# Optimization experiments

Measured on AMD Instinct MI355X. Metric: run time of the kernel, lower is better.

Reference implementation:

```python
import jax, jax.numpy as jnp
import numpy as np

B, T, L, D = 512, 100, 256, 128
DEPTH = 8                 # perfect binary tree depth -> path length DEPTH+1
P = DEPTH + 1
N_PER_TREE = 2 * L - 1    # 511 nodes per tree (heap layout)
N_TOTAL = T * N_PER_TREE  # 51100 global nodes


def _build_paths():
    # Heap layout per tree: internal nodes 0..L-2, leaves L-1..2L-2.
    # Path for leaf l = chain of heap ancestors from root to leaf.
    local = np.zeros((L, P), dtype=np.int32)
    for l in range(L):
        node = L - 1 + l
        chain = []
        while True:
            chain.append(node)
            if node == 0:
                break
            node = (node - 1) // 2
        local[l] = np.array(chain[::-1], dtype=np.int32)
    offs = (np.arange(T, dtype=np.int32) * N_PER_TREE)[:, None, None]
    return local[None, :, :] + offs  # [T, L, P] global node ids


def setup_inputs() -> dict:
    key = jax.random.key(0)
    k1, k2, k3, k4, k5, k6 = jax.random.split(key, 6)
    paths = jnp.asarray(_build_paths())
    # GBDT multi-hot: exactly one activated leaf per tree per sample
    leaf = jax.random.randint(k1, (B, T), 0, L)
    cross = (jnp.zeros((B, T, L), jnp.float32)
             .at[jnp.arange(B)[:, None], jnp.arange(T)[None, :], leaf]
             .set(1.0)
             .reshape(B, T * L))
    s = 1.0 / float(np.sqrt(D))  # torch LSTM init range
    node_emb = jax.random.normal(k2, (N_TOTAL, D), jnp.float32) * 0.01
    w_ih = jax.random.uniform(k3, (4 * D, D), jnp.float32, -s, s)
    w_hh = jax.random.uniform(k4, (4 * D, D), jnp.float32, -s, s)
    b_ih = jax.random.uniform(k5, (4 * D,), jnp.float32, -s, s)
    b_hh = jax.random.uniform(k6, (4 * D,), jnp.float32, -s, s)
    return {"cross_features": cross, "node_emb": node_emb, "w_ih": w_ih,
            "w_hh": w_hh, "b_ih": b_ih, "b_hh": b_hh, "paths": paths}


def _lstm_last_h(x, w_ih, w_hh, b_ih, b_hh):
    # x: [S, P, D] -> final hidden state [S, D]; torch gate order i, f, g, o
    S = x.shape[0]
    d = w_hh.shape[1]
    bias = b_ih + b_hh

    def step(carry, x_t):
        h, c = carry
        g = x_t @ w_ih.T + h @ w_hh.T + bias          # [S, 4D]
        i, f, gg, o = jnp.split(g, 4, axis=-1)
        c = jax.nn.sigmoid(f) * c + jax.nn.sigmoid(i) * jnp.tanh(gg)
        h = jax.nn.sigmoid(o) * jnp.tanh(c)
        return (h, c), None

    h0 = jnp.zeros((S, d), x.dtype)
    (h, _), _ = jax.lax.scan(step, (h0, h0), jnp.swapaxes(x, 0, 1))
    return h


def reference(cross_features, node_emb, w_ih, w_hh, b_ih, b_hh, paths):
    t, l, p = paths.shape
    b = cross_features.shape[0]
    d = node_emb.shape[1]
    cf = cross_features.reshape(b, t, l)
    leaf = jnp.argmax(cf, axis=-1)                    # [B, T] activated leaf per tree
    active = jnp.any(cf > 0, axis=-1)                 # [B, T] tree has an activated leaf
    node_ids = paths[jnp.arange(t)[None, :], leaf]    # [B, T, P] root-to-leaf global ids
    x = node_emb[node_ids].reshape(b * t, p, d)       # batched path gather
    h = _lstm_last_h(x, w_ih, w_hh, b_ih, b_hh).reshape(b, t, d)
    return jnp.where(active[..., None], h, jnp.zeros((), h.dtype))
```

## Files before the change

kernel.cpp:

```cpp
#include <hip/hip_runtime.h>
#include <math.h>


#define B_N 512
#define T_N 100
#define L_N 256
#define D_N 128
#define NPT 511

typedef __attribute__((ext_vector_type(8))) short short8;
typedef __attribute__((ext_vector_type(4))) float f32x4;
typedef __attribute__((ext_vector_type(4))) unsigned short ushort4v;

__device__ __forceinline__ unsigned short f2bf(float f) {
    unsigned u = __float_as_uint(f);
    return (unsigned short)((u + 0x7FFFu + ((u >> 16) & 1u)) >> 16);
}
__device__ __forceinline__ float bf2f(unsigned short b) {
    return __uint_as_float(((unsigned)b) << 16);
}
__device__ __forceinline__ float fsigmoid(float x) {
    return __builtin_amdgcn_rcpf(1.f + __builtin_amdgcn_exp2f(-1.44269504f * x));
}
__device__ __forceinline__ float ftanh(float x) {
    return 1.f - 2.f * __builtin_amdgcn_rcpf(1.f + __builtin_amdgcn_exp2f(2.88539009f * x));
}
__device__ __forceinline__ void keepreg(short8 &x) {
    asm volatile("" : "+v"(x));
}

__global__ __launch_bounds__(256) void pack_kernel(const float* __restrict__ w_ih,
                                                   const float* __restrict__ w_hh,
                                                   const float* __restrict__ b_ih,
                                                   const float* __restrict__ b_hh,
                                                   unsigned short* __restrict__ Bhi,
                                                   unsigned short* __restrict__ Blo,
                                                   float* __restrict__ bias) {
    const int idx = blockIdx.x * 256 + threadIdx.x;
    const int k  = idx & 255;
    const int np = idx >> 8;
    const float val = (k < 128) ? w_ih[(size_t)np * 128 + k]
                                : w_hh[(size_t)np * 128 + (k - 128)];
    const unsigned short hi = f2bf(val);
    const int kb = k >> 5, krel = k & 31, quad = krel >> 3, e = krel & 7;
    const int tn = np >> 4, col = np & 15, lane = quad * 16 + col;
    Bhi[(((size_t)kb * 32 + tn) * 64 + lane) * 8 + e] = hi;
    if (kb >= 4) {
        const unsigned short lo = f2bf(val - bf2f(hi));
        Blo[((((size_t)kb - 4) * 32 + tn) * 64 + lane) * 8 + e] = lo;
    }
    if (k == 0) bias[np] = b_ih[np] + b_hh[np];
}

__global__ __launch_bounds__(512, 2) void tree_kernel(
    const float* __restrict__ node_emb,
    const unsigned short* __restrict__ Bhi,
    const unsigned short* __restrict__ Blo,
    const float* __restrict__ bias,
    float* __restrict__ h8)
{
    __shared__ float hbuf[2][16][132];
    __shared__ float cbuf[2][16][132];
    __shared__ float h7buf[32][132];
    __shared__ float c7buf[32][132];
    __shared__ unsigned short AhiF[8 * 2 * 512];
    __shared__ unsigned short AloF[4 * 2 * 512];

    const int t    = blockIdx.x >> 2;
    const int s    = blockIdx.x & 3;
    const int tid  = threadIdx.x;
    const int idx  = tid >> 6;
    const int lane = tid & 63;
    const int ml   = lane & 15;
    const int quad = lane >> 4;
    const int j    = idx * 16 + ml;

    const float bi = bias[j];
    const float bf = bias[128 + j];
    const float bg = bias[256 + j];
    const float bo = bias[384 + j];

    const short8* Bh8 = reinterpret_cast<const short8*>(Bhi);
    const short8* Bl8 = reinterpret_cast<const short8*>(Blo);
    const short8* Ah8 = reinterpret_cast<const short8*>(AhiF);
    const short8* Al8 = reinterpret_cast<const short8*>(AloF);

    short8 bhR[8][4], blR[4][4];
    #pragma unroll
    for (int kb = 0; kb < 8; ++kb)
        #pragma unroll
        for (int g = 0; g < 4; ++g)
            bhR[kb][g] = Bh8[(kb * 32 + g * 8 + idx) * 64 + lane];
    #pragma unroll
    for (int kb = 0; kb < 4; ++kb)
        #pragma unroll
        for (int g = 0; g < 4; ++g)
            blR[kb][g] = Bl8[(kb * 32 + g * 8 + idx) * 64 + lane];
    #pragma unroll
    for (int kb = 0; kb < 8; ++kb)
        #pragma unroll
        for (int g = 0; g < 4; ++g)
            keepreg(bhR[kb][g]);
    #pragma unroll
    for (int kb = 0; kb < 4; ++kb)
        #pragma unroll
        for (int g = 0; g < 4; ++g)
            keepreg(blR[kb][g]);

    for (int d = 0; d <= 6; ++d) {
        const int Mrows = (d == 0) ? 1 : (d == 1) ? 2 : (1 << (d - 2));
        const int pbase = (d >= 2) ? (s << (d - 2)) : 0;
        const bool root = (d == 0);
        const int cur = d & 1, prv = cur ^ 1;

        #pragma unroll
        for (int h2 = 0; h2 < 2; ++h2) {
            const int r  = tid & 15;
            const int k4 = (tid >> 4) + h2 * 32;
            const int k  = k4 * 4;
            int p = r; if (p > Mrows - 1) p = Mrows - 1;
            float4 v;
            if (k < 128) {
                const int local = (1 << d) - 1 + pbase + p;
                v = *reinterpret_cast<const float4*>(
                        node_emb + (size_t)(t * NPT + local) * D_N + k);
            } else if (root) {
                v = make_float4(0.f, 0.f, 0.f, 0.f);
            } else {
                const int pr = (d == 2) ? (s >> 1) : (p >> 1);
                v = *reinterpret_cast<const float4*>(&hbuf[prv][pr][k - 128]);
            }
            const int kb = k >> 5, qk = (k & 31) >> 3, e0 = k & 4;
            const ushort4v hv = { f2bf(v.x), f2bf(v.y), f2bf(v.z), f2bf(v.w) };
            *reinterpret_cast<ushort4v*>(
                &AhiF[((kb * 2 + 0) * 64 + qk * 16 + r) * 8 + e0]) = hv;
            if (k >= 128) {
                const ushort4v lv = { f2bf(v.x - bf2f(hv.x)), f2bf(v.y - bf2f(hv.y)),
                                      f2bf(v.z - bf2f(hv.z)), f2bf(v.w - bf2f(hv.w)) };
                *reinterpret_cast<ushort4v*>(
                    &AloF[(((kb - 4) * 2 + 0) * 64 + qk * 16 + r) * 8 + e0]) = lv;
            }
        }
        __syncthreads();

        float cpre[4];
        #pragma unroll
        for (int rr = 0; rr < 4; ++rr) {
            int m = quad * 4 + rr;
            if (m > Mrows - 1) m = Mrows - 1;
            const int pr = (d == 2) ? (s >> 1) : (m >> 1);
            cpre[rr] = root ? 0.f : cbuf[prv][pr][j];
        }

        f32x4 acc[4];
        #pragma unroll
        for (int g = 0; g < 4; ++g) acc[g] = (f32x4)0.f;

        #pragma unroll
        for (int kb = 0; kb < 8; ++kb) {
            const short8 ah = Ah8[(kb * 2 + 0) * 64 + lane];
            short8 al;
            if (kb >= 4) al = Al8[((kb - 4) * 2 + 0) * 64 + lane];
            #pragma unroll
            for (int g = 0; g < 4; ++g) {
                acc[g] = __builtin_amdgcn_mfma_f32_16x16x32_bf16(
                    ah, bhR[kb][g], acc[g], 0, 0, 0);
                if (kb >= 4) {
                    acc[g] = __builtin_amdgcn_mfma_f32_16x16x32_bf16(
                        ah, blR[kb - 4][g], acc[g], 0, 0, 0);
                    acc[g] = __builtin_amdgcn_mfma_f32_16x16x32_bf16(
                        al, bhR[kb][g], acc[g], 0, 0, 0);
                }
            }
        }

        #pragma unroll
        for (int rr = 0; rr < 4; ++rr) {
            const int m = quad * 4 + rr;
            if (m < Mrows) {
                const float ig = fsigmoid(acc[0][rr] + bi);
                const float fg = fsigmoid(acc[1][rr] + bf);
                const float gv = ftanh(acc[2][rr] + bg);
                const float og = fsigmoid(acc[3][rr] + bo);
                const float cn = fg * cpre[rr] + ig * gv;
                const float hn = og * ftanh(cn);
                hbuf[cur][m][j] = hn;
                cbuf[cur][m][j] = cn;
            }
        }
        __syncthreads();
    }

    {
        #pragma unroll
        for (int h2 = 0; h2 < 4; ++h2) {
            const int r  = tid & 31;
            const int k4 = (tid >> 5) + h2 * 16;
            const int k  = k4 * 4;
            const int mt = r >> 4, mlr = r & 15;
            float4 v;
            if (k < 128) {
                const int local = 127 + s * 32 + r;
                v = *reinterpret_cast<const float4*>(
                        node_emb + (size_t)(t * NPT + local) * D_N + k);
            } else {
                v = *reinterpret_cast<const float4*>(&hbuf[0][r >> 1][k - 128]);
            }
            const int kb = k >> 5, qk = (k & 31) >> 3, e0 = k & 4;
            const ushort4v hv = { f2bf(v.x), f2bf(v.y), f2bf(v.z), f2bf(v.w) };
            *reinterpret_cast<ushort4v*>(
                &AhiF[((kb * 2 + mt) * 64 + qk * 16 + mlr) * 8 + e0]) = hv;
            if (k >= 128) {
                const ushort4v lv = { f2bf(v.x - bf2f(hv.x)), f2bf(v.y - bf2f(hv.y)),
                                      f2bf(v.z - bf2f(hv.z)), f2bf(v.w - bf2f(hv.w)) };
                *reinterpret_cast<ushort4v*>(
                    &AloF[(((kb - 4) * 2 + mt) * 64 + qk * 16 + mlr) * 8 + e0]) = lv;
            }
        }
        __syncthreads();

        #pragma unroll
        for (int mt = 0; mt < 2; ++mt) {
            float cpre[4];
            #pragma unroll
            for (int rr = 0; rr < 4; ++rr) {
                const int m = mt * 16 + quad * 4 + rr;
                cpre[rr] = cbuf[0][m >> 1][j];
            }
            f32x4 acc[4];
            #pragma unroll
            for (int g = 0; g < 4; ++g) acc[g] = (f32x4)0.f;
            #pragma unroll
            for (int kb = 0; kb < 8; ++kb) {
                const short8 ah = Ah8[(kb * 2 + mt) * 64 + lane];
                short8 al;
                if (kb >= 4) al = Al8[((kb - 4) * 2 + mt) * 64 + lane];
                #pragma unroll
                for (int g = 0; g < 4; ++g) {
                    acc[g] = __builtin_amdgcn_mfma_f32_16x16x32_bf16(
                        ah, bhR[kb][g], acc[g], 0, 0, 0);
                    if (kb >= 4) {
                        acc[g] = __builtin_amdgcn_mfma_f32_16x16x32_bf16(
                            ah, blR[kb - 4][g], acc[g], 0, 0, 0);
                        acc[g] = __builtin_amdgcn_mfma_f32_16x16x32_bf16(
                            al, bhR[kb][g], acc[g], 0, 0, 0);
                    }
                }
            }
            #pragma unroll
            for (int rr = 0; rr < 4; ++rr) {
                const int m = mt * 16 + quad * 4 + rr;
                const float ig = fsigmoid(acc[0][rr] + bi);
                const float fg = fsigmoid(acc[1][rr] + bf);
                const float gv = ftanh(acc[2][rr] + bg);
                const float og = fsigmoid(acc[3][rr] + bo);
                const float cn = fg * cpre[rr] + ig * gv;
                const float hn = og * ftanh(cn);
                h7buf[m][j] = hn;
                c7buf[m][j] = cn;
            }
        }
        __syncthreads();
    }

    for (int pp = 0; pp < 2; ++pp) {
        #pragma unroll
        for (int h2 = 0; h2 < 4; ++h2) {
            const int r  = tid & 31;
            const int m2 = pp * 32 + r;
            const int k4 = (tid >> 5) + h2 * 16;
            const int k  = k4 * 4;
            const int mt = r >> 4, mlr = r & 15;
            float4 v;
            if (k < 128) {
                const int local = 255 + s * 64 + m2;
                v = *reinterpret_cast<const float4*>(
                        node_emb + (size_t)(t * NPT + local) * D_N + k);
            } else {
                v = *reinterpret_cast<const float4*>(&h7buf[m2 >> 1][k - 128]);
            }
            const int kb = k >> 5, qk = (k & 31) >> 3, e0 = k & 4;
            const ushort4v hv = { f2bf(v.x), f2bf(v.y), f2bf(v.z), f2bf(v.w) };
            *reinterpret_cast<ushort4v*>(
                &AhiF[((kb * 2 + mt) * 64 + qk * 16 + mlr) * 8 + e0]) = hv;
            if (k >= 128) {
                const ushort4v lv = { f2bf(v.x - bf2f(hv.x)), f2bf(v.y - bf2f(hv.y)),
                                      f2bf(v.z - bf2f(hv.z)), f2bf(v.w - bf2f(hv.w)) };
                *reinterpret_cast<ushort4v*>(
                    &AloF[(((kb - 4) * 2 + mt) * 64 + qk * 16 + mlr) * 8 + e0]) = lv;
            }
        }
        __syncthreads();

        #pragma unroll
        for (int mt = 0; mt < 2; ++mt) {
            float cpre[4];
            #pragma unroll
            for (int rr = 0; rr < 4; ++rr) {
                const int m2 = pp * 32 + mt * 16 + quad * 4 + rr;
                cpre[rr] = c7buf[m2 >> 1][j];
            }
            f32x4 acc[4];
            #pragma unroll
            for (int g = 0; g < 4; ++g) acc[g] = (f32x4)0.f;
            #pragma unroll
            for (int kb = 0; kb < 8; ++kb) {
                const short8 ah = Ah8[(kb * 2 + mt) * 64 + lane];
                short8 al;
                if (kb >= 4) al = Al8[((kb - 4) * 2 + mt) * 64 + lane];
                #pragma unroll
                for (int g = 0; g < 4; ++g) {
                    acc[g] = __builtin_amdgcn_mfma_f32_16x16x32_bf16(
                        ah, bhR[kb][g], acc[g], 0, 0, 0);
                    if (kb >= 4) {
                        acc[g] = __builtin_amdgcn_mfma_f32_16x16x32_bf16(
                            ah, blR[kb - 4][g], acc[g], 0, 0, 0);
                        acc[g] = __builtin_amdgcn_mfma_f32_16x16x32_bf16(
                            al, bhR[kb][g], acc[g], 0, 0, 0);
                    }
                }
            }
            #pragma unroll
            for (int rr = 0; rr < 4; ++rr) {
                const int m2 = pp * 32 + mt * 16 + quad * 4 + rr;
                const float ig = fsigmoid(acc[0][rr] + bi);
                const float fg = fsigmoid(acc[1][rr] + bf);
                const float gv = ftanh(acc[2][rr] + bg);
                const float og = fsigmoid(acc[3][rr] + bo);
                const float cn = fg * cpre[rr] + ig * gv;
                const float hn = og * ftanh(cn);
                h8[(size_t)((t << 8) + s * 64 + m2) * D_N + j] = hn;
            }
        }
        __syncthreads();
    }
}

__global__ __launch_bounds__(256) void gather_kernel(const float* __restrict__ cross,
                                                     const float* __restrict__ h8,
                                                     float* __restrict__ out) {
    const int bt   = blockIdx.x * 4 + (threadIdx.x >> 6);
    const int lane = threadIdx.x & 63;
    const int t    = bt % T_N;
    const float4 v = reinterpret_cast<const float4*>(cross + (size_t)bt * L_N)[lane];
    int idx = -1;
    if      (v.x > 0.f) idx = lane * 4 + 0;
    else if (v.y > 0.f) idx = lane * 4 + 1;
    else if (v.z > 0.f) idx = lane * 4 + 2;
    else if (v.w > 0.f) idx = lane * 4 + 3;
    const unsigned long long m = __ballot(idx >= 0);
    int lf = -1;
    if (m != 0ULL) {
        const int first = __builtin_ctzll(m);
        lf = __shfl(idx, first);
    }
    float2 o = make_float2(0.f, 0.f);
    if (lf >= 0)
        o = reinterpret_cast<const float2*>(h8 + (size_t)(t * L_N + lf) * D_N)[lane];
    reinterpret_cast<float2*>(out + (size_t)bt * D_N)[lane] = o;
}

extern "C" void kernel_launch(void* const* d_in, const int* in_sizes, int n_in,
                              void* d_out, int out_size, void* d_ws, size_t ws_size,
                              hipStream_t stream) {
    const float* cross    = (const float*)d_in[0];
    const float* node_emb = (const float*)d_in[1];
    const float* w_ih     = (const float*)d_in[2];
    const float* w_hh     = (const float*)d_in[3];
    const float* b_ih     = (const float*)d_in[4];
    const float* b_hh     = (const float*)d_in[5];
    float* out = (float*)d_out;
    float* ws  = (float*)d_ws;

    float* h8   = ws;
    float* bias = h8 + (size_t)51200 * D_N;
    unsigned short* Bhi = (unsigned short*)(bias + 512);
    unsigned short* Blo = Bhi + 131072;

    pack_kernel<<<512, 256, 0, stream>>>(w_ih, w_hh, b_ih, b_hh, Bhi, Blo, bias);

    tree_kernel<<<4 * T_N, 512, 0, stream>>>(node_emb, Bhi, Blo, bias, h8);

    gather_kernel<<<(B_N * T_N) / 4, 256, 0, stream>>>(cross, h8, out);
}
```

Baseline: 188.4 us.

## Process two trees per block to halve grid and reuse register-held weights

```diff
diff --git a/kernel.cpp b/kernel.cpp
--- a/kernel.cpp
+++ b/kernel.cpp
@@ -59,21 +59,21 @@
     const float* __restrict__ bias,
     float* __restrict__ h8)
 {
-    __shared__ float hbuf[2][16][132];
-    __shared__ float cbuf[2][16][132];
-    __shared__ float h7buf[32][132];
-    __shared__ float c7buf[32][132];
-    __shared__ unsigned short AhiF[8 * 2 * 512];
-    __shared__ unsigned short AloF[4 * 2 * 512];
-
-    const int t    = blockIdx.x >> 2;
+    __shared__ float hbuf[2][2][16][132];
+    __shared__ float cbuf[2][2][16][132];
+    __shared__ float h7buf[2][32][132];
+    __shared__ unsigned short AhiF[8 * 4 * 512];
+    __shared__ unsigned short AloF[4 * 4 * 512];
+
+    const int tp   = blockIdx.x >> 2;
     const int s    = blockIdx.x & 3;
+    const int t0   = tp * 2;
     const int tid  = threadIdx.x;
-    const int idx  = tid >> 6;
+    const int widx = tid >> 6;
     const int lane = tid & 63;
     const int ml   = lane & 15;
     const int quad = lane >> 4;
-    const int j    = idx * 16 + ml;
+    const int j    = widx * 16 + ml;
 
     const float bi = bias[j];
     const float bf = bias[128 + j];
@@ -90,12 +90,12 @@
     for (int kb = 0; kb < 8; ++kb)
         #pragma unroll
         for (int g = 0; g < 4; ++g)
-            bhR[kb][g] = Bh8[(kb * 32 + g * 8 + idx) * 64 + lane];
+            bhR[kb][g] = Bh8[(kb * 32 + g * 8 + widx) * 64 + lane];
     #pragma unroll
     for (int kb = 0; kb < 4; ++kb)
         #pragma unroll
         for (int g = 0; g < 4; ++g)
-            blR[kb][g] = Bl8[(kb * 32 + g * 8 + idx) * 64 + lane];
+            blR[kb][g] = Bl8[(kb * 32 + g * 8 + widx) * 64 + lane];
     #pragma unroll
     for (int kb = 0; kb < 8; ++kb)
         #pragma unroll
@@ -114,222 +114,237 @@
         const int cur = d & 1, prv = cur ^ 1;
 
         #pragma unroll
-        for (int h2 = 0; h2 < 2; ++h2) {
-            const int r  = tid & 15;
-            const int k4 = (tid >> 4) + h2 * 32;
+        for (int h2 = 0; h2 < 4; ++h2) {
+            const int r5 = tid & 31;
+            const int u  = r5 >> 4, r = r5 & 15;
+            const int k4 = (tid >> 5) + h2 * 16;
             const int k  = k4 * 4;
             int p = r; if (p > Mrows - 1) p = Mrows - 1;
             float4 v;
             if (k < 128) {
                 const int local = (1 << d) - 1 + pbase + p;
                 v = *reinterpret_cast<const float4*>(
-                        node_emb + (size_t)(t * NPT + local) * D_N + k);
+                        node_emb + (size_t)((t0 + u) * NPT + local) * D_N + k);
             } else if (root) {
                 v = make_float4(0.f, 0.f, 0.f, 0.f);
             } else {
                 const int pr = (d == 2) ? (s >> 1) : (p >> 1);
-                v = *reinterpret_cast<const float4*>(&hbuf[prv][pr][k - 128]);
+                v = *reinterpret_cast<const float4*>(&hbuf[prv][u][pr][k - 128]);
             }
             const int kb = k >> 5, qk = (k & 31) >> 3, e0 = k & 4;
             const ushort4v hv = { f2bf(v.x), f2bf(v.y), f2bf(v.z), f2bf(v.w) };
             *reinterpret_cast<ushort4v*>(
-                &AhiF[((kb * 2 + 0) * 64 + qk * 16 + r) * 8 + e0]) = hv;
+                &AhiF[((kb * 4 + u) * 64 + qk * 16 + r) * 8 + e0]) = hv;
             if (k >= 128) {
                 const ushort4v lv = { f2bf(v.x - bf2f(hv.x)), f2bf(v.y - bf2f(hv.y)),
                                       f2bf(v.z - bf2f(hv.z)), f2bf(v.w - bf2f(hv.w)) };
                 *reinterpret_cast<ushort4v*>(
-                    &AloF[(((kb - 4) * 2 + 0) * 64 + qk * 16 + r) * 8 + e0]) = lv;
-            }
-        }
-        __syncthreads();
-
-        float cpre[4];
-        #pragma unroll
-        for (int rr = 0; rr < 4; ++rr) {
-            int m = quad * 4 + rr;
-            if (m > Mrows - 1) m = Mrows - 1;
-            const int pr = (d == 2) ? (s >> 1) : (m >> 1);
-            cpre[rr] = root ? 0.f : cbuf[prv][pr][j];
-        }
-
-        f32x4 acc[4];
-        #pragma unroll
-        for (int g = 0; g < 4; ++g) acc[g] = (f32x4)0.f;
-
-        #pragma unroll
-        for (int kb = 0; kb < 8; ++kb) {
-            const short8 ah = Ah8[(kb * 2 + 0) * 64 + lane];
-            short8 al;
-            if (kb >= 4) al = Al8[((kb - 4) * 2 + 0) * 64 + lane];
-            #pragma unroll
-            for (int g = 0; g < 4; ++g) {
-                acc[g] = __builtin_amdgcn_mfma_f32_16x16x32_bf16(
-                    ah, bhR[kb][g], acc[g], 0, 0, 0);
-                if (kb >= 4) {
+                    &AloF[(((kb - 4) * 4 + u) * 64 + qk * 16 + r) * 8 + e0]) = lv;
+            }
+        }
+        __syncthreads();
+
+        #pragma unroll
+        for (int u = 0; u < 2; ++u) {
+            float cpre[4];
+            #pragma unroll
+            for (int rr = 0; rr < 4; ++rr) {
+                int m = quad * 4 + rr;
+                if (m > Mrows - 1) m = Mrows - 1;
+                const int pr = (d == 2) ? (s >> 1) : (m >> 1);
+                cpre[rr] = root ? 0.f : cbuf[prv][u][pr][j];
+            }
+
+            f32x4 acc[4];
+            #pragma unroll
+            for (int g = 0; g < 4; ++g) acc[g] = (f32x4)0.f;
+
+            #pragma unroll
+            for (int kb = 0; kb < 8; ++kb) {
+                const short8 ah = Ah8[(kb * 4 + u) * 64 + lane];
+                short8 al;
+                if (kb >= 4) al = Al8[((kb - 4) * 4 + u) * 64 + lane];
+                #pragma unroll
+                for (int g = 0; g < 4; ++g) {
                     acc[g] = __builtin_amdgcn_mfma_f32_16x16x32_bf16(
-                        ah, blR[kb - 4][g], acc[g], 0, 0, 0);
+                        ah, bhR[kb][g], acc[g], 0, 0, 0);
+                    if (kb >= 4) {
+                        acc[g] = __builtin_amdgcn_mfma_f32_16x16x32_bf16(
+                            ah, blR[kb - 4][g], acc[g], 0, 0, 0);
+                        acc[g] = __builtin_amdgcn_mfma_f32_16x16x32_bf16(
+                            al, bhR[kb][g], acc[g], 0, 0, 0);
+                    }
+                }
+            }
+
+            #pragma unroll
+            for (int rr = 0; rr < 4; ++rr) {
+                const int m = quad * 4 + rr;
+                if (m < Mrows) {
+                    const float ig = fsigmoid(acc[0][rr] + bi);
+                    const float fg = fsigmoid(acc[1][rr] + bf);
+                    const float gv = ftanh(acc[2][rr] + bg);
+                    const float og = fsigmoid(acc[3][rr] + bo);
+                    const float cn = fg * cpre[rr] + ig * gv;
+                    const float hn = og * ftanh(cn);
+                    hbuf[cur][u][m][j] = hn;
+                    cbuf[cur][u][m][j] = cn;
+                }
+            }
+        }
+        __syncthreads();
+    }
+
+    {
+        #pragma unroll
+        for (int h2 = 0; h2 < 8; ++h2) {
+            const int r6 = tid & 63;
+            const int u  = r6 >> 5, m = r6 & 31;
+            const int k4 = (tid >> 6) + h2 * 8;
+            const int k  = k4 * 4;
+            const int mt = r6 >> 4, mlr = r6 & 15;
+            float4 v;
+            if (k < 128) {
+                const int local = 127 + s * 32 + m;
+                v = *reinterpret_cast<const float4*>(
+                        node_emb + (size_t)((t0 + u) * NPT + local) * D_N + k);
+            } else {
+                v = *reinterpret_cast<const float4*>(&hbuf[0][u][m >> 1][k - 128]);
+            }
+            const int kb = k >> 5, qk = (k & 31) >> 3, e0 = k & 4;
+            const ushort4v hv = { f2bf(v.x), f2bf(v.y), f2bf(v.z), f2bf(v.w) };
+            *reinterpret_cast<ushort4v*>(
+                &AhiF[((kb * 4 + mt) * 64 + qk * 16 + mlr) * 8 + e0]) = hv;
+            if (k >= 128) {
+                const ushort4v lv = { f2bf(v.x - bf2f(hv.x)), f2bf(v.y - bf2f(hv.y)),
+                                      f2bf(v.z - bf2f(hv.z)), f2bf(v.w - bf2f(hv.w)) };
+                *reinterpret_cast<ushort4v*>(
+                    &AloF[(((kb - 4) * 4 + mt) * 64 + qk * 16 + mlr) * 8 + e0]) = lv;
+            }
+        }
+        __syncthreads();
+
+        float cpreA[4][4];
+        #pragma unroll
+        for (int mt = 0; mt < 4; ++mt) {
+            const int u = mt >> 1;
+            #pragma unroll
+            for (int rr = 0; rr < 4; ++rr) {
+                const int m = (mt & 1) * 16 + quad * 4 + rr;
+                cpreA[mt][rr] = cbuf[0][u][m >> 1][j];
+            }
+        }
+        __syncthreads();
+
+        #pragma unroll
+        for (int mt = 0; mt < 4; ++mt) {
+            const int u = mt >> 1;
+            f32x4 acc[4];
+            #pragma unroll
+            for (int g = 0; g < 4; ++g) acc[g] = (f32x4)0.f;
+            #pragma unroll
+            for (int kb = 0; kb < 8; ++kb) {
+                const short8 ah = Ah8[(kb * 4 + mt) * 64 + lane];
+                short8 al;
+                if (kb >= 4) al = Al8[((kb - 4) * 4 + mt) * 64 + lane];
+                #pragma unroll
+                for (int g = 0; g < 4; ++g) {
                     acc[g] = __builtin_amdgcn_mfma_f32_16x16x32_bf16(
-                        al, bhR[kb][g], acc[g], 0, 0, 0);
+                        ah, bhR[kb][g], acc[g], 0, 0, 0);
+                    if (kb >= 4) {
+                        acc[g] = __builtin_amdgcn_mfma_f32_16x16x32_bf16(
+                            ah, blR[kb - 4][g], acc[g], 0, 0, 0);
+                        acc[g] = __builtin_amdgcn_mfma_f32_16x16x32_bf16(
+                            al, bhR[kb][g], acc[g], 0, 0, 0);
+                    }
                 }
             }
-        }
-
-        #pragma unroll
-        for (int rr = 0; rr < 4; ++rr) {
-            const int m = quad * 4 + rr;
-            if (m < Mrows) {
+            #pragma unroll
+            for (int rr = 0; rr < 4; ++rr) {
+                const int m = (mt & 1) * 16 + quad * 4 + rr;
+                const float ig = fsigmoid(acc[0][rr] + bi);
+                const float fg = fsigmoid(acc[1][rr] + bf);
+                const float gv = ftanh(acc[2][rr] + bg);
+                const float og = fsigmoid(acc[3][rr] + bo);
+                const float cn = fg * cpreA[mt][rr] + ig * gv;
+                const float hn = og * ftanh(cn);
+                h7buf[u][m][j] = hn;
+                cbuf[m >> 4][u][m & 15][j] = cn;
+            }
+        }
+        __syncthreads();
+    }
+
+    for (int pp = 0; pp < 2; ++pp) {
+        #pragma unroll
+        for (int h2 = 0; h2 < 8; ++h2) {
+            const int r6   = tid & 63;
+            const int u    = r6 >> 5, m31 = r6 & 31;
+            const int mrow = pp * 32 + m31;
+            const int k4   = (tid >> 6) + h2 * 8;
+            const int k    = k4 * 4;
+            const int mt   = r6 >> 4, mlr = r6 & 15;
+            float4 v;
+            if (k < 128) {
+                const int local = 255 + s * 64 + mrow;
+                v = *reinterpret_cast<const float4*>(
+                        node_emb + (size_t)((t0 + u) * NPT + local) * D_N + k);
+            } else {
+                v = *reinterpret_cast<const float4*>(&h7buf[u][mrow >> 1][k - 128]);
+            }
+            const int kb = k >> 5, qk = (k & 31) >> 3, e0 = k & 4;
+            const ushort4v hv = { f2bf(v.x), f2bf(v.y), f2bf(v.z), f2bf(v.w) };
+            *reinterpret_cast<ushort4v*>(
+                &AhiF[((kb * 4 + mt) * 64 + qk * 16 + mlr) * 8 + e0]) = hv;
+            if (k >= 128) {
+                const ushort4v lv = { f2bf(v.x - bf2f(hv.x)), f2bf(v.y - bf2f(hv.y)),
+                                      f2bf(v.z - bf2f(hv.z)), f2bf(v.w - bf2f(hv.w)) };
+                *reinterpret_cast<ushort4v*>(
+                    &AloF[(((kb - 4) * 4 + mt) * 64 + qk * 16 + mlr) * 8 + e0]) = lv;
+            }
+        }
+        __syncthreads();
+
+        #pragma unroll
+        for (int mt = 0; mt < 4; ++mt) {
+            const int u = mt >> 1;
+            float cpre[4];
+            #pragma unroll
+            for (int rr = 0; rr < 4; ++rr) {
+                const int mrow = pp * 32 + (mt & 1) * 16 + quad * 4 + rr;
+                const int c7r  = mrow >> 1;
+                cpre[rr] = cbuf[c7r >> 4][u][c7r & 15][j];
+            }
+            f32x4 acc[4];
+            #pragma unroll
+            for (int g = 0; g < 4; ++g) acc[g] = (f32x4)0.f;
+            #pragma unroll
+            for (int kb = 0; kb < 8; ++kb) {
+                const short8 ah = Ah8[(kb * 4 + mt) * 64 + lane];
+                short8 al;
+                if (kb >= 4) al = Al8[((kb - 4) * 4 + mt) * 64 + lane];
+                #pragma unroll
+                for (int g = 0; g < 4; ++g) {
+                    acc[g] = __builtin_amdgcn_mfma_f32_16x16x32_bf16(
+                        ah, bhR[kb][g], acc[g], 0, 0, 0);
+                    if (kb >= 4) {
+                        acc[g] = __builtin_amdgcn_mfma_f32_16x16x32_bf16(
+                            ah, blR[kb - 4][g], acc[g], 0, 0, 0);
+                        acc[g] = __builtin_amdgcn_mfma_f32_16x16x32_bf16(
+                            al, bhR[kb][g], acc[g], 0, 0, 0);
+                    }
+                }
+            }
+            #pragma unroll
+            for (int rr = 0; rr < 4; ++rr) {
+                const int mrow = pp * 32 + (mt & 1) * 16 + quad * 4 + rr;
                 const float ig = fsigmoid(acc[0][rr] + bi);
                 const float fg = fsigmoid(acc[1][rr] + bf);
                 const float gv = ftanh(acc[2][rr] + bg);
                 const float og = fsigmoid(acc[3][rr] + bo);
                 const float cn = fg * cpre[rr] + ig * gv;
                 const float hn = og * ftanh(cn);
-                hbuf[cur][m][j] = hn;
-                cbuf[cur][m][j] = cn;
-            }
-        }
-        __syncthreads();
-    }
-
-    {
-        #pragma unroll
-        for (int h2 = 0; h2 < 4; ++h2) {
-            const int r  = tid & 31;
-            const int k4 = (tid >> 5) + h2 * 16;
-            const int k  = k4 * 4;
-            const int mt = r >> 4, mlr = r & 15;
-            float4 v;
-            if (k < 128) {
-                const int local = 127 + s * 32 + r;
-                v = *reinterpret_cast<const float4*>(
-                        node_emb + (size_t)(t * NPT + local) * D_N + k);
-            } else {
-                v = *reinterpret_cast<const float4*>(&hbuf[0][r >> 1][k - 128]);
-            }
-            const int kb = k >> 5, qk = (k & 31) >> 3, e0 = k & 4;
-            const ushort4v hv = { f2bf(v.x), f2bf(v.y), f2bf(v.z), f2bf(v.w) };
-            *reinterpret_cast<ushort4v*>(
-                &AhiF[((kb * 2 + mt) * 64 + qk * 16 + mlr) * 8 + e0]) = hv;
-            if (k >= 128) {
-                const ushort4v lv = { f2bf(v.x - bf2f(hv.x)), f2bf(v.y - bf2f(hv.y)),
-                                      f2bf(v.z - bf2f(hv.z)), f2bf(v.w - bf2f(hv.w)) };
-                *reinterpret_cast<ushort4v*>(
-                    &AloF[(((kb - 4) * 2 + mt) * 64 + qk * 16 + mlr) * 8 + e0]) = lv;
-            }
-        }
-        __syncthreads();
-
-        #pragma unroll
-        for (int mt = 0; mt < 2; ++mt) {
-            float cpre[4];
-            #pragma unroll
-            for (int rr = 0; rr < 4; ++rr) {
-                const int m = mt * 16 + quad * 4 + rr;
-                cpre[rr] = cbuf[0][m >> 1][j];
-            }
-            f32x4 acc[4];
-            #pragma unroll
-            for (int g = 0; g < 4; ++g) acc[g] = (f32x4)0.f;
-            #pragma unroll
-            for (int kb = 0; kb < 8; ++kb) {
-                const short8 ah = Ah8[(kb * 2 + mt) * 64 + lane];
-                short8 al;
-                if (kb >= 4) al = Al8[((kb - 4) * 2 + mt) * 64 + lane];
-                #pragma unroll
-                for (int g = 0; g < 4; ++g) {
-                    acc[g] = __builtin_amdgcn_mfma_f32_16x16x32_bf16(
-                        ah, bhR[kb][g], acc[g], 0, 0, 0);
-                    if (kb >= 4) {
-                        acc[g] = __builtin_amdgcn_mfma_f32_16x16x32_bf16(
-                            ah, blR[kb - 4][g], acc[g], 0, 0, 0);
-                        acc[g] = __builtin_amdgcn_mfma_f32_16x16x32_bf16(
-                            al, bhR[kb][g], acc[g], 0, 0, 0);
-                    }
-                }
-            }
-            #pragma unroll
-            for (int rr = 0; rr < 4; ++rr) {
-                const int m = mt * 16 + quad * 4 + rr;
-                const float ig = fsigmoid(acc[0][rr] + bi);
-                const float fg = fsigmoid(acc[1][rr] + bf);
-                const float gv = ftanh(acc[2][rr] + bg);
-                const float og = fsigmoid(acc[3][rr] + bo);
-                const float cn = fg * cpre[rr] + ig * gv;
-                const float hn = og * ftanh(cn);
-                h7buf[m][j] = hn;
-                c7buf[m][j] = cn;
-            }
-        }
-        __syncthreads();
-    }
-
-    for (int pp = 0; pp < 2; ++pp) {
-        #pragma unroll
-        for (int h2 = 0; h2 < 4; ++h2) {
-            const int r  = tid & 31;
-            const int m2 = pp * 32 + r;
-            const int k4 = (tid >> 5) + h2 * 16;
-            const int k  = k4 * 4;
-            const int mt = r >> 4, mlr = r & 15;
-            float4 v;
-            if (k < 128) {
-                const int local = 255 + s * 64 + m2;
-                v = *reinterpret_cast<const float4*>(
-                        node_emb + (size_t)(t * NPT + local) * D_N + k);
-            } else {
-                v = *reinterpret_cast<const float4*>(&h7buf[m2 >> 1][k - 128]);
-            }
-            const int kb = k >> 5, qk = (k & 31) >> 3, e0 = k & 4;
-            const ushort4v hv = { f2bf(v.x), f2bf(v.y), f2bf(v.z), f2bf(v.w) };
-            *reinterpret_cast<ushort4v*>(
-                &AhiF[((kb * 2 + mt) * 64 + qk * 16 + mlr) * 8 + e0]) = hv;
-            if (k >= 128) {
-                const ushort4v lv = { f2bf(v.x - bf2f(hv.x)), f2bf(v.y - bf2f(hv.y)),
-                                      f2bf(v.z - bf2f(hv.z)), f2bf(v.w - bf2f(hv.w)) };
-                *reinterpret_cast<ushort4v*>(
-                    &AloF[(((kb - 4) * 2 + mt) * 64 + qk * 16 + mlr) * 8 + e0]) = lv;
-            }
-        }
-        __syncthreads();
-
-        #pragma unroll
-        for (int mt = 0; mt < 2; ++mt) {
-            float cpre[4];
-            #pragma unroll
-            for (int rr = 0; rr < 4; ++rr) {
-                const int m2 = pp * 32 + mt * 16 + quad * 4 + rr;
-                cpre[rr] = c7buf[m2 >> 1][j];
-            }
-            f32x4 acc[4];
-            #pragma unroll
-            for (int g = 0; g < 4; ++g) acc[g] = (f32x4)0.f;
-            #pragma unroll
-            for (int kb = 0; kb < 8; ++kb) {
-                const short8 ah = Ah8[(kb * 2 + mt) * 64 + lane];
-                short8 al;
-                if (kb >= 4) al = Al8[((kb - 4) * 2 + mt) * 64 + lane];
-                #pragma unroll
-                for (int g = 0; g < 4; ++g) {
-                    acc[g] = __builtin_amdgcn_mfma_f32_16x16x32_bf16(
-                        ah, bhR[kb][g], acc[g], 0, 0, 0);
-                    if (kb >= 4) {
-                        acc[g] = __builtin_amdgcn_mfma_f32_16x16x32_bf16(
-                            ah, blR[kb - 4][g], acc[g], 0, 0, 0);
-                        acc[g] = __builtin_amdgcn_mfma_f32_16x16x32_bf16(
-                            al, bhR[kb][g], acc[g], 0, 0, 0);
-                    }
-                }
-            }
-            #pragma unroll
-            for (int rr = 0; rr < 4; ++rr) {
-                const int m2 = pp * 32 + mt * 16 + quad * 4 + rr;
-                const float ig = fsigmoid(acc[0][rr] + bi);
-                const float fg = fsigmoid(acc[1][rr] + bf);
-                const float gv = ftanh(acc[2][rr] + bg);
-                const float og = fsigmoid(acc[3][rr] + bo);
-                const float cn = fg * cpre[rr] + ig * gv;
-                const float hn = og * ftanh(cn);
-                h8[(size_t)((t << 8) + s * 64 + m2) * D_N + j] = hn;
+                h8[(size_t)(((t0 + u) << 8) + s * 64 + mrow) * D_N + j] = hn;
             }
         }
         __syncthreads();
@@ -379,7 +394,7 @@
 
     pack_kernel<<<512, 256, 0, stream>>>(w_ih, w_hh, b_ih, b_hh, Bhi, Blo, bias);
 
-    tree_kernel<<<4 * T_N, 512, 0, stream>>>(node_emb, Bhi, Blo, bias, h8);
+    tree_kernel<<<(T_N / 2) * 4, 512, 0, stream>>>(node_emb, Bhi, Blo, bias, h8);
 
     gather_kernel<<<(B_N * T_N) / 4, 256, 0, stream>>>(cross, h8, out);
 }
```

Result: slower. 198.2 us (+5.2%).
